# Performance work log

Hardware: AMD Instinct MI355X
Metric: run time of the kernel (lower is better)

The kernel has to match this reference:

```python
import jax, jax.numpy as jnp
import numpy as np

NREF, NALT, B, D, F = 131072, 32768, 4096, 128, 512
H = F // 2  # d_ffn // 2
EPS = 1e-5


def _ln(x, w, b):
    m = jnp.mean(x, axis=-1, keepdims=True)
    v = jnp.mean((x - m) ** 2, axis=-1, keepdims=True)
    return (x - m) * jax.lax.rsqrt(v + EPS) * w + b


def setup_inputs() -> dict:
    key = jax.random.key(0)
    ks = jax.random.split(key, 16)
    s = 0.02
    return {
        "ref_flat": jax.random.normal(ks[0], (NREF, D), jnp.float32),
        "alt_flat": jax.random.normal(ks[1], (NALT, D), jnp.float32),
        "ref_seg": jnp.sort(jax.random.randint(ks[2], (NREF,), 0, B)),
        "alt_seg": jnp.sort(jax.random.randint(ks[3], (NALT,), 0, B)),
        "norm1_w": jnp.ones((D,), jnp.float32),
        "norm1_b": jnp.zeros((D,), jnp.float32),
        "w1_ref": jax.random.normal(ks[4], (D, F), jnp.float32) * s,
        "b1_ref": jnp.zeros((F,), jnp.float32),
        "w1_alt": jax.random.normal(ks[5], (D, F), jnp.float32) * s,
        "b1_alt": jnp.zeros((F,), jnp.float32),
        "norm2_w": jnp.ones((H,), jnp.float32),
        "norm2_b": jnp.zeros((H,), jnp.float32),
        "alpha_ref": jnp.float32(0.01),
        "alpha_alt": jnp.float32(0.01),
        "beta_ref": jnp.float32(0.01),
        "beta_alt": jnp.float32(0.01),
        "gamma": jnp.float32(0.01),
        "ref_regularizer": 0.1 * jnp.ones((H,), jnp.float32),
        "reg_w_pre": jnp.float32(np.log(0.1)),
        "w2_ref": jax.random.normal(ks[6], (H, D), jnp.float32) * s,
        "b2_ref": jnp.zeros((D,), jnp.float32),
        "w2_alt": jax.random.normal(ks[7], (H, D), jnp.float32) * s,
        "b2_alt": jnp.zeros((D,), jnp.float32),
    }


def reference(ref_flat, alt_flat, ref_seg, alt_seg,
              norm1_w, norm1_b, w1_ref, b1_ref, w1_alt, b1_alt,
              norm2_w, norm2_b, alpha_ref, alpha_alt, beta_ref, beta_alt,
              gamma, ref_regularizer, reg_w_pre, w2_ref, b2_ref, w2_alt, b2_alt):
    # proj1 + SELU on flattened ragged reads
    zr = jax.nn.selu(_ln(ref_flat, norm1_w, norm1_b) @ w1_ref + b1_ref)   # [NREF, F]
    za = jax.nn.selu(_ln(alt_flat, norm1_w, norm1_b) @ w1_alt + b1_alt)   # [NALT, F]
    z1r, z2r = zr[:, :H], zr[:, H:]
    z1a, z2a = za[:, :H], za[:, H:]
    z2r = _ln(z2r, norm2_w, norm2_b)
    z2a = _ln(z2a, norm2_w, norm2_b)

    cnt_r = jax.ops.segment_sum(jnp.ones((NREF,), z2r.dtype), ref_seg, num_segments=B)
    cnt_a = jax.ops.segment_sum(jnp.ones((NALT,), z2a.dtype), alt_seg, num_segments=B)
    reg_w = jnp.exp(reg_w_pre) + 0.25
    # regularized mean field over each ref set
    ref_mf = (jax.ops.segment_sum(z2r, ref_seg, num_segments=B)
              + reg_w * ref_regularizer) / (cnt_r[:, None] + reg_w)       # [B, H]
    alt_mf = jax.ops.segment_sum(z2a, alt_seg, num_segments=B) \
             / jnp.maximum(cnt_a, 1.0)[:, None]                            # [B, H]

    ref_gate = z2r * alpha_ref + 1.0 + (beta_ref * ref_mf)[ref_seg]
    alt_gate = z2a * alpha_alt + 1.0 + (beta_alt * alt_mf + gamma * ref_mf)[alt_seg]

    out_r = ref_flat + (z1r * ref_gate) @ w2_ref + b2_ref
    out_a = alt_flat + (z1a * alt_gate) @ w2_alt + b2_alt
    return out_r, out_a
```

## Files before the change

### kernel.cpp

```cpp
#include <hip/hip_runtime.h>
#include <hip/hip_bf16.h>

#define NREF 131072
#define NALT 32768
#define BSEG 4096
#define D 128
#define F 512
#define H 256
#define EPS 1e-5f
#define NB_REF 4096
#define NB_ALT 1024

typedef short short8 __attribute__((ext_vector_type(8)));
typedef float f32x4 __attribute__((ext_vector_type(4)));

__device__ __forceinline__ float selu_f(float z) {
    const float sc = 1.0507009873554805f;
    const float al = 1.6732632423543772f;
    return z > 0.f ? sc * z : sc * al * (__expf(z) - 1.f);
}

__device__ __forceinline__ short f2bf(float v) {
    __bf16 b = (__bf16)v;
    return __builtin_bit_cast(short, b);
}

__device__ __forceinline__ float bf2f(short s) {
    return (float)__builtin_bit_cast(__bf16, s);
}

__global__ void prep_kernel(const float* __restrict__ w1_ref, const float* __restrict__ w1_alt,
                            const float* __restrict__ w2_ref, const float* __restrict__ w2_alt,
                            __bf16* __restrict__ w1p_r, __bf16* __restrict__ w1p_a,
                            __bf16* __restrict__ w2p_r, __bf16* __restrict__ w2p_a,
                            float* __restrict__ zbase) {
    int b = blockIdx.x;
    if (b < 768) {
        const float* w; __bf16* wp; int KT, N, idx;
        if (b < 256)      { w = w1_ref; wp = w1p_r; KT = 4; N = F; idx = b * 256 + threadIdx.x; }
        else if (b < 512) { w = w1_alt; wp = w1p_a; KT = 4; N = F; idx = (b - 256) * 256 + threadIdx.x; }
        else if (b < 640) { w = w2_ref; wp = w2p_r; KT = 8; N = D; idx = (b - 512) * 256 + threadIdx.x; }
        else              { w = w2_alt; wp = w2p_a; KT = 8; N = D; idx = (b - 640) * 256 + threadIdx.x; }
        int j = idx & 7;
        int l = (idx >> 3) & 63;
        int t = idx >> 9;
        int kt = t % KT;
        int nt = t / KT;
        int k = kt * 32 + ((l >> 4) << 3) + j;
        int n = (nt << 4) + (l & 15);
        wp[idx] = (__bf16)w[k * N + n];
    } else {
        int t = (b - 768) * 256 + threadIdx.x;
        float4 z = {0.f, 0.f, 0.f, 0.f};
        for (int i = t; i < 526336; i += 512 * 256)
            reinterpret_cast<float4*>(zbase)[i] = z;
    }
}

__global__ __launch_bounds__(256, 4)
void pass1_kernel(const float* __restrict__ xr_, const float* __restrict__ xa_,
                  const int* __restrict__ segr_, const int* __restrict__ sega_,
                  const __bf16* __restrict__ w1pr_, const __bf16* __restrict__ w1pa_,
                  const float* __restrict__ b1r_, const float* __restrict__ b1a_,
                  const float* __restrict__ n1w, const float* __restrict__ n1b,
                  const float* __restrict__ n2w, const float* __restrict__ n2b,
                  float* __restrict__ sumr_, float* __restrict__ cntr_,
                  float* __restrict__ suma_, float* __restrict__ cnta_,
                  __bf16* __restrict__ z2nr_, __bf16* __restrict__ z2na_,
                  int boff) {
    __shared__ __align__(16) __bf16 ys[32 * 128];
    __shared__ __align__(16) __bf16 z2s[32 * 256];
    __shared__ float n2w_s[H], n2b_s[H];
    __shared__ int seg_s[32];

    const int b = blockIdx.x + boff;
    const float* x; const int* seg; const __bf16* w1p; const float* b1;
    float* seg_sum; float* seg_cnt; __bf16* z2n_out; size_t row0;
    if (b < NB_REF) {
        x = xr_; seg = segr_; w1p = w1pr_; b1 = b1r_;
        seg_sum = sumr_; seg_cnt = cntr_; z2n_out = z2nr_;
        row0 = (size_t)b * 32;
    } else {
        x = xa_; seg = sega_; w1p = w1pa_; b1 = b1a_;
        seg_sum = suma_; seg_cnt = cnta_; z2n_out = z2na_;
        row0 = (size_t)(b - NB_REF) * 32;
    }

    const int tid = threadIdx.x;
    const int lane = tid & 63;
    const int wv = tid >> 6;
    const int q = lane >> 4, m0 = lane & 15;

    short8 bb[2][4];
    #pragma unroll
    for (int p = 0; p < 2; ++p)
        #pragma unroll
        for (int kt = 0; kt < 4; ++kt)
            bb[p][kt] = *reinterpret_cast<const short8*>(
                w1p + ((size_t)((16 + wv * 4 + p) * 4 + kt) * 64 + lane) * 8);
    float b1v[4];
    #pragma unroll
    for (int nt = 0; nt < 4; ++nt) b1v[nt] = b1[256 + (wv * 4 + nt) * 16 + m0];

    const int r = tid >> 3, g = tid & 7;
    float xr[16];
    #pragma unroll
    for (int i = 0; i < 4; ++i) {
        float4 t = *reinterpret_cast<const float4*>(x + (row0 + r) * D + g * 16 + i * 4);
        xr[i * 4 + 0] = t.x; xr[i * 4 + 1] = t.y; xr[i * 4 + 2] = t.z; xr[i * 4 + 3] = t.w;
    }
    float w1r[16], c1r[16];
    #pragma unroll
    for (int i = 0; i < 4; ++i) {
        float4 t = *reinterpret_cast<const float4*>(n1w + g * 16 + i * 4);
        w1r[i * 4 + 0] = t.x; w1r[i * 4 + 1] = t.y; w1r[i * 4 + 2] = t.z; w1r[i * 4 + 3] = t.w;
        float4 u = *reinterpret_cast<const float4*>(n1b + g * 16 + i * 4);
        c1r[i * 4 + 0] = u.x; c1r[i * 4 + 1] = u.y; c1r[i * 4 + 2] = u.z; c1r[i * 4 + 3] = u.w;
    }

    n2w_s[tid] = n2w[tid]; n2b_s[tid] = n2b[tid];
    if (tid < 32) seg_s[tid] = seg[row0 + tid];

    {
        float s = 0.f, ss = 0.f;
        #pragma unroll
        for (int i = 0; i < 16; ++i) { s += xr[i]; ss += xr[i] * xr[i]; }
        s += __shfl_xor(s, 1); ss += __shfl_xor(ss, 1);
        s += __shfl_xor(s, 2); ss += __shfl_xor(ss, 2);
        s += __shfl_xor(s, 4); ss += __shfl_xor(ss, 4);
        float mean = s * (1.f / 128.f);
        float var = ss * (1.f / 128.f) - mean * mean;
        float rsv = rsqrtf(var + EPS);
        const int swr = (r & 7) << 3;
        #pragma unroll
        for (int h = 0; h < 2; ++h) {
            short8 pk;
            #pragma unroll
            for (int j = 0; j < 8; ++j)
                pk[j] = f2bf((xr[h * 8 + j] - mean) * rsv * w1r[h * 8 + j] + c1r[h * 8 + j]);
            *reinterpret_cast<short8*>(&ys[r * 128 + ((g * 16 + h * 8) ^ swr)]) = pk;
        }
    }
    __syncthreads();

    {
        const int swm = (m0 & 7) << 3;
        const int ccol = q << 3;
        short8 a0[4], a1[4];
        #pragma unroll
        for (int kt = 0; kt < 4; ++kt) {
            a0[kt] = *reinterpret_cast<const short8*>(&ys[m0 * 128 + ((kt * 32 + ccol) ^ swm)]);
            a1[kt] = *reinterpret_cast<const short8*>(&ys[(m0 + 16) * 128 + ((kt * 32 + ccol) ^ swm)]);
        }
        #pragma unroll
        for (int nt = 0; nt < 4; ++nt) {
            f32x4 acc0 = {0.f, 0.f, 0.f, 0.f};
            f32x4 acc1 = {0.f, 0.f, 0.f, 0.f};
            #pragma unroll
            for (int kt = 0; kt < 4; ++kt) {
                acc0 = __builtin_amdgcn_mfma_f32_16x16x32_bf16(a0[kt], bb[nt & 1][kt], acc0, 0, 0, 0);
                acc1 = __builtin_amdgcn_mfma_f32_16x16x32_bf16(a1[kt], bb[nt & 1][kt], acc1, 0, 0, 0);
            }
            if (nt < 2) {
                #pragma unroll
                for (int kt = 0; kt < 4; ++kt)
                    bb[nt & 1][kt] = *reinterpret_cast<const short8*>(
                        w1p + ((size_t)((16 + wv * 4 + nt + 2) * 4 + kt) * 64 + lane) * 8);
            }
            int cz = (wv * 4 + nt) * 16 + m0;
            #pragma unroll
            for (int reg = 0; reg < 4; ++reg) {
                int r0 = (q << 2) + reg;
                int r1 = r0 + 16;
                z2s[r0 * 256 + (cz ^ ((r0 & 7) << 3))] = (__bf16)selu_f(acc0[reg] + b1v[nt]);
                z2s[r1 * 256 + (cz ^ ((r1 & 7) << 3))] = (__bf16)selu_f(acc1[reg] + b1v[nt]);
            }
        }
    }
    __syncthreads();

    {
        const int swr = (r & 7) << 3;
        float vb[32];
        float s2 = 0.f, q2 = 0.f;
        #pragma unroll
        for (int i = 0; i < 4; ++i) {
            short8 v = *reinterpret_cast<const short8*>(&z2s[r * 256 + ((g * 32 + i * 8) ^ swr)]);
            #pragma unroll
            for (int j = 0; j < 8; ++j) {
                float f = bf2f(v[j]);
                vb[i * 8 + j] = f; s2 += f; q2 += f * f;
            }
        }
        s2 += __shfl_xor(s2, 1); q2 += __shfl_xor(q2, 1);
        s2 += __shfl_xor(s2, 2); q2 += __shfl_xor(q2, 2);
        s2 += __shfl_xor(s2, 4); q2 += __shfl_xor(q2, 4);
        float mean2 = s2 * (1.f / 256.f);
        float var2 = q2 * (1.f / 256.f) - mean2 * mean2;
        float rs2 = rsqrtf(var2 + EPS);
        #pragma unroll
        for (int i = 0; i < 4; ++i) {
            short8 o;
            #pragma unroll
            for (int j = 0; j < 8; ++j) {
                int col = g * 32 + i * 8 + j;
                o[j] = f2bf((vb[i * 8 + j] - mean2) * rs2 * n2w_s[col] + n2b_s[col]);
            }
            *reinterpret_cast<short8*>(&z2s[r * 256 + ((g * 32 + i * 8) ^ swr)]) = o;
            *reinterpret_cast<short8*>(z2n_out + (row0 + r) * H + g * 32 + i * 8) = o;
        }
    }
    __syncthreads();

    {
        int c = tid;
        int s_cur = seg_s[0];
        float run = 0.f;
        for (int rr = 0; rr < 32; ++rr) {
            int sg = seg_s[rr];
            if (sg != s_cur) {
                atomicAdd(&seg_sum[(size_t)s_cur * H + c], run);
                run = 0.f; s_cur = sg;
            }
            run += (float)z2s[rr * 256 + (c ^ ((rr & 7) << 3))];
        }
        atomicAdd(&seg_sum[(size_t)s_cur * H + c], run);
        if (tid == 0) {
            int sc = seg_s[0]; float rl = 0.f;
            for (int rr = 0; rr < 32; ++rr) {
                if (seg_s[rr] != sc) { atomicAdd(&seg_cnt[sc], rl); rl = 0.f; sc = seg_s[rr]; }
                rl += 1.f;
            }
            atomicAdd(&seg_cnt[sc], rl);
        }
    }
}

__global__ void mf_kernel(const float* __restrict__ sum_r, const float* __restrict__ cnt_r,
                          const float* __restrict__ sum_a, const float* __restrict__ cnt_a,
                          const float* __restrict__ regz, const float* __restrict__ reg_w_pre,
                          const float* __restrict__ beta_ref, const float* __restrict__ beta_alt,
                          const float* __restrict__ gamma,
                          float* __restrict__ G_ref, float* __restrict__ G_alt) {
    int s = blockIdx.x, c = threadIdx.x;
    size_t i = (size_t)s * H + c;
    float rw = __expf(reg_w_pre[0]) + 0.25f;
    float mfr = (sum_r[i] + rw * regz[c]) / (cnt_r[s] + rw);
    float mfa = sum_a[i] / fmaxf(cnt_a[s], 1.f);
    G_ref[i] = beta_ref[0] * mfr;
    G_alt[i] = beta_alt[0] * mfa + gamma[0] * mfr;
}

__global__ __launch_bounds__(256, 4)
void pass2_kernel(const float* __restrict__ xr_, const float* __restrict__ xa_,
                  const int* __restrict__ segr_, const int* __restrict__ sega_,
                  const __bf16* __restrict__ w1pr_, const __bf16* __restrict__ w1pa_,
                  const float* __restrict__ b1r_, const float* __restrict__ b1a_,
                  const __bf16* __restrict__ w2pr_, const __bf16* __restrict__ w2pa_,
                  const float* __restrict__ b2r_, const float* __restrict__ b2a_,
                  const float* __restrict__ n1w, const float* __restrict__ n1b,
                  const float* __restrict__ alphar_, const float* __restrict__ alphaa_,
                  const float* __restrict__ Gr_, const float* __restrict__ Ga_,
                  const __bf16* __restrict__ z2nr_, const __bf16* __restrict__ z2na_,
                  float* __restrict__ out_, int boff) {
    __shared__ __align__(16) __bf16 ys[32 * 128];
    __shared__ __align__(16) __bf16 zs[32 * 256];

    const int b = blockIdx.x + boff;
    const float* x; const int* seg; const __bf16* w1p; const float* b1;
    const __bf16* w2p; const float* b2; const float* alpha_p; const float* G;
    const __bf16* z2n; float* out; size_t row0;
    if (b < NB_REF) {
        x = xr_; seg = segr_; w1p = w1pr_; b1 = b1r_; w2p = w2pr_; b2 = b2r_;
        alpha_p = alphar_; G = Gr_; z2n = z2nr_; out = out_;
        row0 = (size_t)b * 32;
    } else {
        x = xa_; seg = sega_; w1p = w1pa_; b1 = b1a_; w2p = w2pa_; b2 = b2a_;
        alpha_p = alphaa_; G = Ga_; z2n = z2na_; out = out_ + (size_t)NREF * D;
        row0 = (size_t)(b - NB_REF) * 32;
    }

    const int tid = threadIdx.x;
    const int lane = tid & 63;
    const int wv = tid >> 6;
    const int q = lane >> 4, m0 = lane & 15;
    const int r = tid >> 3, g = tid & 7;

    short8 bb[2][4];
    #pragma unroll
    for (int p = 0; p < 2; ++p)
        #pragma unroll
        for (int kt = 0; kt < 4; ++kt)
            bb[p][kt] = *reinterpret_cast<const short8*>(
                w1p + ((size_t)((wv * 4 + p) * 4 + kt) * 64 + lane) * 8);
    float b1v[4];
    #pragma unroll
    for (int nt = 0; nt < 4; ++nt) b1v[nt] = b1[(wv * 4 + nt) * 16 + m0];

    const int segi = seg[row0 + r];
    const float alpha = alpha_p[0];

    float xr[16];
    #pragma unroll
    for (int i = 0; i < 4; ++i) {
        float4 t = *reinterpret_cast<const float4*>(x + (row0 + r) * D + g * 16 + i * 4);
        xr[i * 4 + 0] = t.x; xr[i * 4 + 1] = t.y; xr[i * 4 + 2] = t.z; xr[i * 4 + 3] = t.w;
    }
    float w1r[16], c1r[16];
    #pragma unroll
    for (int i = 0; i < 4; ++i) {
        float4 t = *reinterpret_cast<const float4*>(n1w + g * 16 + i * 4);
        w1r[i * 4 + 0] = t.x; w1r[i * 4 + 1] = t.y; w1r[i * 4 + 2] = t.z; w1r[i * 4 + 3] = t.w;
        float4 u = *reinterpret_cast<const float4*>(n1b + g * 16 + i * 4);
        c1r[i * 4 + 0] = u.x; c1r[i * 4 + 1] = u.y; c1r[i * 4 + 2] = u.z; c1r[i * 4 + 3] = u.w;
    }

    {
        float s = 0.f, ss = 0.f;
        #pragma unroll
        for (int i = 0; i < 16; ++i) { s += xr[i]; ss += xr[i] * xr[i]; }
        s += __shfl_xor(s, 1); ss += __shfl_xor(ss, 1);
        s += __shfl_xor(s, 2); ss += __shfl_xor(ss, 2);
        s += __shfl_xor(s, 4); ss += __shfl_xor(ss, 4);
        float mean = s * (1.f / 128.f);
        float var = ss * (1.f / 128.f) - mean * mean;
        float rsv = rsqrtf(var + EPS);
        const int swr = (r & 7) << 3;
        #pragma unroll
        for (int h = 0; h < 2; ++h) {
            short8 pk;
            #pragma unroll
            for (int j = 0; j < 8; ++j)
                pk[j] = f2bf((xr[h * 8 + j] - mean) * rsv * w1r[h * 8 + j] + c1r[h * 8 + j]);
            *reinterpret_cast<short8*>(&ys[r * 128 + ((g * 16 + h * 8) ^ swr)]) = pk;
        }
    }
    __syncthreads();

    {
        const int swm = (m0 & 7) << 3;
        const int ccol = q << 3;
        short8 a0[4], a1[4];
        #pragma unroll
        for (int kt = 0; kt < 4; ++kt) {
            a0[kt] = *reinterpret_cast<const short8*>(&ys[m0 * 128 + ((kt * 32 + ccol) ^ swm)]);
            a1[kt] = *reinterpret_cast<const short8*>(&ys[(m0 + 16) * 128 + ((kt * 32 + ccol) ^ swm)]);
        }
        #pragma unroll
        for (int nt = 0; nt < 4; ++nt) {
            f32x4 acc0 = {0.f, 0.f, 0.f, 0.f};
            f32x4 acc1 = {0.f, 0.f, 0.f, 0.f};
            #pragma unroll
            for (int kt = 0; kt < 4; ++kt) {
                acc0 = __builtin_amdgcn_mfma_f32_16x16x32_bf16(a0[kt], bb[nt & 1][kt], acc0, 0, 0, 0);
                acc1 = __builtin_amdgcn_mfma_f32_16x16x32_bf16(a1[kt], bb[nt & 1][kt], acc1, 0, 0, 0);
            }
            if (nt < 2) {
                #pragma unroll
                for (int kt = 0; kt < 4; ++kt)
                    bb[nt & 1][kt] = *reinterpret_cast<const short8*>(
                        w1p + ((size_t)((wv * 4 + nt + 2) * 4 + kt) * 64 + lane) * 8);
            }
            int cz = (wv * 4 + nt) * 16 + m0;
            #pragma unroll
            for (int reg = 0; reg < 4; ++reg) {
                int r0 = (q << 2) + reg;
                int r1 = r0 + 16;
                zs[r0 * 256 + (cz ^ ((r0 & 7) << 3))] = (__bf16)selu_f(acc0[reg] + b1v[nt]);
                zs[r1 * 256 + (cz ^ ((r1 & 7) << 3))] = (__bf16)selu_f(acc1[reg] + b1v[nt]);
            }
        }
    }

    short8 zn[4];
    #pragma unroll
    for (int i = 0; i < 4; ++i)
        zn[i] = *reinterpret_cast<const short8*>(z2n + (row0 + r) * H + g * 32 + i * 8);
    float gvf[32];
    {
        const float* Gp = G + (size_t)segi * H + g * 32;
        #pragma unroll
        for (int i = 0; i < 8; ++i) {
            float4 t = *reinterpret_cast<const float4*>(Gp + i * 4);
            gvf[i * 4 + 0] = t.x; gvf[i * 4 + 1] = t.y; gvf[i * 4 + 2] = t.z; gvf[i * 4 + 3] = t.w;
        }
    }
    short8 b2f[2][8];
    #pragma unroll
    for (int p = 0; p < 2; ++p)
        #pragma unroll
        for (int kt = 0; kt < 8; ++kt)
            b2f[p][kt] = *reinterpret_cast<const short8*>(
                w2p + ((size_t)((wv * 2 + p) * 8 + kt) * 64 + lane) * 8);
    float b2v[2];
    #pragma unroll
    for (int p = 0; p < 2; ++p) b2v[p] = b2[(wv * 2 + p) * 16 + m0];
    __syncthreads();

    {
        const int swr = (r & 7) << 3;
        #pragma unroll
        for (int i = 0; i < 4; ++i) {
            int idx = r * 256 + ((g * 32 + i * 8) ^ swr);
            short8 v = *reinterpret_cast<const short8*>(&zs[idx]);
            short8 o;
            #pragma unroll
            for (int j = 0; j < 8; ++j) {
                float gate = bf2f(zn[i][j]) * alpha + 1.f + gvf[i * 8 + j];
                o[j] = f2bf(bf2f(v[j]) * gate);
            }
            *reinterpret_cast<short8*>(&zs[idx]) = o;
        }
    }
    float xres[16];
    #pragma unroll
    for (int p = 0; p < 2; ++p) {
        int col = (wv * 2 + p) * 16 + m0;
        #pragma unroll
        for (int reg = 0; reg < 4; ++reg) {
            int r0 = (q << 2) + reg;
            xres[p * 8 + reg]     = x[(row0 + r0) * D + col];
            xres[p * 8 + 4 + reg] = x[(row0 + r0 + 16) * D + col];
        }
    }
    __syncthreads();

    {
        const int swm = (m0 & 7) << 3;
        const int ccol = q << 3;
        f32x4 zero = {0.f, 0.f, 0.f, 0.f};
        f32x4 acc[2][2] = {{zero, zero}, {zero, zero}};
        #pragma unroll
        for (int kt = 0; kt < 8; ++kt) {
            short8 a0 = *reinterpret_cast<const short8*>(&zs[m0 * 256 + ((kt * 32 + ccol) ^ swm)]);
            short8 a1 = *reinterpret_cast<const short8*>(&zs[(m0 + 16) * 256 + ((kt * 32 + ccol) ^ swm)]);
            #pragma unroll
            for (int p = 0; p < 2; ++p) {
                acc[p][0] = __builtin_amdgcn_mfma_f32_16x16x32_bf16(a0, b2f[p][kt], acc[p][0], 0, 0, 0);
                acc[p][1] = __builtin_amdgcn_mfma_f32_16x16x32_bf16(a1, b2f[p][kt], acc[p][1], 0, 0, 0);
            }
        }
        #pragma unroll
        for (int p = 0; p < 2; ++p) {
            int col = (wv * 2 + p) * 16 + m0;
            #pragma unroll
            for (int reg = 0; reg < 4; ++reg) {
                int r0 = (q << 2) + reg;
                out[(row0 + r0) * D + col]      = acc[p][0][reg] + b2v[p] + xres[p * 8 + reg];
                out[(row0 + r0 + 16) * D + col] = acc[p][1][reg] + b2v[p] + xres[p * 8 + 4 + reg];
            }
        }
    }
}

extern "C" void kernel_launch(void* const* d_in, const int* in_sizes, int n_in,
                              void* d_out, int out_size, void* d_ws, size_t ws_size,
                              hipStream_t stream) {
    const float* ref_flat = (const float*)d_in[0];
    const float* alt_flat = (const float*)d_in[1];
    const int*   ref_seg  = (const int*)d_in[2];
    const int*   alt_seg  = (const int*)d_in[3];
    const float* norm1_w  = (const float*)d_in[4];
    const float* norm1_b  = (const float*)d_in[5];
    const float* w1_ref   = (const float*)d_in[6];
    const float* b1_ref   = (const float*)d_in[7];
    const float* w1_alt   = (const float*)d_in[8];
    const float* b1_alt   = (const float*)d_in[9];
    const float* norm2_w  = (const float*)d_in[10];
    const float* norm2_b  = (const float*)d_in[11];
    const float* alpha_ref = (const float*)d_in[12];
    const float* alpha_alt = (const float*)d_in[13];
    const float* beta_ref  = (const float*)d_in[14];
    const float* beta_alt  = (const float*)d_in[15];
    const float* gamma     = (const float*)d_in[16];
    const float* ref_regularizer = (const float*)d_in[17];
    const float* reg_w_pre = (const float*)d_in[18];
    const float* w2_ref   = (const float*)d_in[19];
    const float* b2_ref   = (const float*)d_in[20];
    const float* w2_alt   = (const float*)d_in[21];
    const float* b2_alt   = (const float*)d_in[22];

    char* ws = (char*)d_ws;
    float* sum_r = (float*)(ws);
    float* sum_a = (float*)(ws + 4194304);
    float* cnt_r = (float*)(ws + 8388608);
    float* cnt_a = (float*)(ws + 8404992);
    float* G_ref = (float*)(ws + 8421376);
    float* G_alt = (float*)(ws + 12615680);
    __bf16* w1p_r = (__bf16*)(ws + 16809984);
    __bf16* w1p_a = (__bf16*)(ws + 16941056);
    __bf16* w2p_r = (__bf16*)(ws + 17072128);
    __bf16* w2p_a = (__bf16*)(ws + 17137664);
    __bf16* z2n_r = (__bf16*)(ws + 17203200);
    __bf16* z2n_a = (__bf16*)(ws + 84312064);

    const bool merged = ws_size >= (size_t)101089280;
    if (!merged) z2n_a = z2n_r;

    prep_kernel<<<1280, 256, 0, stream>>>(w1_ref, w1_alt, w2_ref, w2_alt,
                                          w1p_r, w1p_a, w2p_r, w2p_a, (float*)ws);

    if (merged) {
        pass1_kernel<<<NB_REF + NB_ALT, 256, 0, stream>>>(
            ref_flat, alt_flat, ref_seg, alt_seg, w1p_r, w1p_a, b1_ref, b1_alt,
            norm1_w, norm1_b, norm2_w, norm2_b,
            sum_r, cnt_r, sum_a, cnt_a, z2n_r, z2n_a, 0);
        mf_kernel<<<BSEG, 256, 0, stream>>>(sum_r, cnt_r, sum_a, cnt_a,
                                            ref_regularizer, reg_w_pre,
                                            beta_ref, beta_alt, gamma, G_ref, G_alt);
        pass2_kernel<<<NB_REF + NB_ALT, 256, 0, stream>>>(
            ref_flat, alt_flat, ref_seg, alt_seg, w1p_r, w1p_a, b1_ref, b1_alt,
            w2p_r, w2p_a, b2_ref, b2_alt, norm1_w, norm1_b,
            alpha_ref, alpha_alt, G_ref, G_alt, z2n_r, z2n_a, (float*)d_out, 0);
    } else {
        pass1_kernel<<<NB_REF, 256, 0, stream>>>(
            ref_flat, alt_flat, ref_seg, alt_seg, w1p_r, w1p_a, b1_ref, b1_alt,
            norm1_w, norm1_b, norm2_w, norm2_b,
            sum_r, cnt_r, sum_a, cnt_a, z2n_r, z2n_a, 0);
        mf_kernel<<<BSEG, 256, 0, stream>>>(sum_r, cnt_r, sum_a, cnt_a,
                                            ref_regularizer, reg_w_pre,
                                            beta_ref, beta_alt, gamma, G_ref, G_alt);
        pass2_kernel<<<NB_REF, 256, 0, stream>>>(
            ref_flat, alt_flat, ref_seg, alt_seg, w1p_r, w1p_a, b1_ref, b1_alt,
            w2p_r, w2p_a, b2_ref, b2_alt, norm1_w, norm1_b,
            alpha_ref, alpha_alt, G_ref, G_alt, z2n_r, z2n_a, (float*)d_out, 0);
        pass1_kernel<<<NB_ALT, 256, 0, stream>>>(
            ref_flat, alt_flat, ref_seg, alt_seg, w1p_r, w1p_a, b1_ref, b1_alt,
            norm1_w, norm1_b, norm2_w, norm2_b,
            sum_r, cnt_r, sum_a, cnt_a, z2n_r, z2n_a, NB_REF);
        mf_kernel<<<BSEG, 256, 0, stream>>>(sum_r, cnt_r, sum_a, cnt_a,
                                            ref_regularizer, reg_w_pre,
                                            beta_ref, beta_alt, gamma, G_ref, G_alt);
        pass2_kernel<<<NB_ALT, 256, 0, stream>>>(
            ref_flat, alt_flat, ref_seg, alt_seg, w1p_r, w1p_a, b1_ref, b1_alt,
            w2p_r, w2p_a, b2_ref, b2_alt, norm1_w, norm1_b,
            alpha_ref, alpha_alt, G_ref, G_alt, z2n_r, z2n_a, (float*)d_out, NB_REF);
    }
}
```

Before: 300.3 us.

## Fuse mean-field kernel into pass2 and raise occupancy launch bounds

Removes the separate mf_kernel launch and computes the per-segment gate term inside pass2 directly from the segment sums, counts and regularizer. This drops one kernel launch plus the writes and reads of the two B×H G buffers, and shrinks the workspace. In exchange, each pass2 thread does extra loads and arithmetic: sum_r and regz for every row, and sum_a too for alt rows. Launch bounds for pass1 and pass2 also go from 4 to 6 waves-per-EU target, which may force register spills.

```diff
diff --git a/kernel.cpp b/kernel.cpp
--- a/kernel.cpp
+++ b/kernel.cpp
@@ -57,7 +57,7 @@
     }
 }
 
-__global__ __launch_bounds__(256, 4)
+__global__ __launch_bounds__(256, 6)
 void pass1_kernel(const float* __restrict__ xr_, const float* __restrict__ xa_,
                   const int* __restrict__ segr_, const int* __restrict__ sega_,
                   const __bf16* __restrict__ w1pr_, const __bf16* __restrict__ w1pa_,
@@ -236,22 +236,7 @@
     }
 }
 
-__global__ void mf_kernel(const float* __restrict__ sum_r, const float* __restrict__ cnt_r,
-                          const float* __restrict__ sum_a, const float* __restrict__ cnt_a,
-                          const float* __restrict__ regz, const float* __restrict__ reg_w_pre,
-                          const float* __restrict__ beta_ref, const float* __restrict__ beta_alt,
-                          const float* __restrict__ gamma,
-                          float* __restrict__ G_ref, float* __restrict__ G_alt) {
-    int s = blockIdx.x, c = threadIdx.x;
-    size_t i = (size_t)s * H + c;
-    float rw = __expf(reg_w_pre[0]) + 0.25f;
-    float mfr = (sum_r[i] + rw * regz[c]) / (cnt_r[s] + rw);
-    float mfa = sum_a[i] / fmaxf(cnt_a[s], 1.f);
-    G_ref[i] = beta_ref[0] * mfr;
-    G_alt[i] = beta_alt[0] * mfa + gamma[0] * mfr;
-}
-
-__global__ __launch_bounds__(256, 4)
+__global__ __launch_bounds__(256, 6)
 void pass2_kernel(const float* __restrict__ xr_, const float* __restrict__ xa_,
                   const int* __restrict__ segr_, const int* __restrict__ sega_,
                   const __bf16* __restrict__ w1pr_, const __bf16* __restrict__ w1pa_,
@@ -260,23 +245,28 @@
                   const float* __restrict__ b2r_, const float* __restrict__ b2a_,
                   const float* __restrict__ n1w, const float* __restrict__ n1b,
                   const float* __restrict__ alphar_, const float* __restrict__ alphaa_,
-                  const float* __restrict__ Gr_, const float* __restrict__ Ga_,
+                  const float* __restrict__ sum_r, const float* __restrict__ cnt_r,
+                  const float* __restrict__ sum_a, const float* __restrict__ cnt_a,
+                  const float* __restrict__ regz, const float* __restrict__ reg_w_pre,
+                  const float* __restrict__ beta_ref_p, const float* __restrict__ beta_alt_p,
+                  const float* __restrict__ gamma_p,
                   const __bf16* __restrict__ z2nr_, const __bf16* __restrict__ z2na_,
                   float* __restrict__ out_, int boff) {
     __shared__ __align__(16) __bf16 ys[32 * 128];
     __shared__ __align__(16) __bf16 zs[32 * 256];
 
     const int b = blockIdx.x + boff;
+    const bool isref = (b < NB_REF);
     const float* x; const int* seg; const __bf16* w1p; const float* b1;
-    const __bf16* w2p; const float* b2; const float* alpha_p; const float* G;
+    const __bf16* w2p; const float* b2; const float* alpha_p;
     const __bf16* z2n; float* out; size_t row0;
-    if (b < NB_REF) {
+    if (isref) {
         x = xr_; seg = segr_; w1p = w1pr_; b1 = b1r_; w2p = w2pr_; b2 = b2r_;
-        alpha_p = alphar_; G = Gr_; z2n = z2nr_; out = out_;
+        alpha_p = alphar_; z2n = z2nr_; out = out_;
         row0 = (size_t)b * 32;
     } else {
         x = xa_; seg = sega_; w1p = w1pa_; b1 = b1a_; w2p = w2pa_; b2 = b2a_;
-        alpha_p = alphaa_; G = Ga_; z2n = z2na_; out = out_ + (size_t)NREF * D;
+        alpha_p = alphaa_; z2n = z2na_; out = out_ + (size_t)NREF * D;
         row0 = (size_t)(b - NB_REF) * 32;
     }
 
@@ -299,6 +289,10 @@
 
     const int segi = seg[row0 + r];
     const float alpha = alpha_p[0];
+    const float rw = __expf(reg_w_pre[0]) + 0.25f;
+    const float bref = beta_ref_p[0];
+    const float balt = beta_alt_p[0];
+    const float gmma = gamma_p[0];
 
     float xr[16];
     #pragma unroll
@@ -378,11 +372,32 @@
         zn[i] = *reinterpret_cast<const short8*>(z2n + (row0 + r) * H + g * 32 + i * 8);
     float gvf[32];
     {
-        const float* Gp = G + (size_t)segi * H + g * 32;
-        #pragma unroll
-        for (int i = 0; i < 8; ++i) {
-            float4 t = *reinterpret_cast<const float4*>(Gp + i * 4);
-            gvf[i * 4 + 0] = t.x; gvf[i * 4 + 1] = t.y; gvf[i * 4 + 2] = t.z; gvf[i * 4 + 3] = t.w;
+        const float invr = 1.f / (cnt_r[segi] + rw);
+        const float* srow = sum_r + (size_t)segi * H + g * 32;
+        const float* rz = regz + g * 32;
+        if (isref) {
+            #pragma unroll
+            for (int i = 0; i < 8; ++i) {
+                float4 s4 = *reinterpret_cast<const float4*>(srow + i * 4);
+                float4 r4 = *reinterpret_cast<const float4*>(rz + i * 4);
+                gvf[i * 4 + 0] = bref * ((s4.x + rw * r4.x) * invr);
+                gvf[i * 4 + 1] = bref * ((s4.y + rw * r4.y) * invr);
+                gvf[i * 4 + 2] = bref * ((s4.z + rw * r4.z) * invr);
+                gvf[i * 4 + 3] = bref * ((s4.w + rw * r4.w) * invr);
+            }
+        } else {
+            const float inva = 1.f / fmaxf(cnt_a[segi], 1.f);
+            const float* sarow = sum_a + (size_t)segi * H + g * 32;
+            #pragma unroll
+            for (int i = 0; i < 8; ++i) {
+                float4 s4 = *reinterpret_cast<const float4*>(srow + i * 4);
+                float4 r4 = *reinterpret_cast<const float4*>(rz + i * 4);
+                float4 a4 = *reinterpret_cast<const float4*>(sarow + i * 4);
+                gvf[i * 4 + 0] = balt * (a4.x * inva) + gmma * ((s4.x + rw * r4.x) * invr);
+                gvf[i * 4 + 1] = balt * (a4.y * inva) + gmma * ((s4.y + rw * r4.y) * invr);
+                gvf[i * 4 + 2] = balt * (a4.z * inva) + gmma * ((s4.z + rw * r4.z) * invr);
+                gvf[i * 4 + 3] = balt * (a4.w * inva) + gmma * ((s4.w + rw * r4.w) * invr);
+            }
         }
     }
     short8 b2f[2][8];
@@ -485,16 +500,14 @@
     float* sum_a = (float*)(ws + 4194304);
     float* cnt_r = (float*)(ws + 8388608);
     float* cnt_a = (float*)(ws + 8404992);
-    float* G_ref = (float*)(ws + 8421376);
-    float* G_alt = (float*)(ws + 12615680);
-    __bf16* w1p_r = (__bf16*)(ws + 16809984);
-    __bf16* w1p_a = (__bf16*)(ws + 16941056);
-    __bf16* w2p_r = (__bf16*)(ws + 17072128);
-    __bf16* w2p_a = (__bf16*)(ws + 17137664);
-    __bf16* z2n_r = (__bf16*)(ws + 17203200);
-    __bf16* z2n_a = (__bf16*)(ws + 84312064);
-
-    const bool merged = ws_size >= (size_t)101089280;
+    __bf16* w1p_r = (__bf16*)(ws + 8421376);
+    __bf16* w1p_a = (__bf16*)(ws + 8552448);
+    __bf16* w2p_r = (__bf16*)(ws + 8683520);
+    __bf16* w2p_a = (__bf16*)(ws + 8749056);
+    __bf16* z2n_r = (__bf16*)(ws + 8814592);
+    __bf16* z2n_a = (__bf16*)(ws + 75923456);
+
+    const bool merged = ws_size >= (size_t)92700672;
     if (!merged) z2n_a = z2n_r;
 
     prep_kernel<<<1280, 256, 0, stream>>>(w1_ref, w1_alt, w2_ref, w2_alt,
@@ -505,35 +518,35 @@
             ref_flat, alt_flat, ref_seg, alt_seg, w1p_r, w1p_a, b1_ref, b1_alt,
             norm1_w, norm1_b, norm2_w, norm2_b,
             sum_r, cnt_r, sum_a, cnt_a, z2n_r, z2n_a, 0);
-        mf_kernel<<<BSEG, 256, 0, stream>>>(sum_r, cnt_r, sum_a, cnt_a,
-                                            ref_regularizer, reg_w_pre,
-                                            beta_ref, beta_alt, gamma, G_ref, G_alt);
         pass2_kernel<<<NB_REF + NB_ALT, 256, 0, stream>>>(
             ref_flat, alt_flat, ref_seg, alt_seg, w1p_r, w1p_a, b1_ref, b1_alt,
             w2p_r, w2p_a, b2_ref, b2_alt, norm1_w, norm1_b,
-            alpha_ref, alpha_alt, G_ref, G_alt, z2n_r, z2n_a, (float*)d_out, 0);
+            alpha_ref, alpha_alt,
+            sum_r, cnt_r, sum_a, cnt_a, ref_regularizer, reg_w_pre,
+            beta_ref, beta_alt, gamma,
+            z2n_r, z2n_a, (float*)d_out, 0);
     } else {
         pass1_kernel<<<NB_REF, 256, 0, stream>>>(
             ref_flat, alt_flat, ref_seg, alt_seg, w1p_r, w1p_a, b1_ref, b1_alt,
             norm1_w, norm1_b, norm2_w, norm2_b,
             sum_r, cnt_r, sum_a, cnt_a, z2n_r, z2n_a, 0);
-        mf_kernel<<<BSEG, 256, 0, stream>>>(sum_r, cnt_r, sum_a, cnt_a,
-                                            ref_regularizer, reg_w_pre,
-                                            beta_ref, beta_alt, gamma, G_ref, G_alt);
         pass2_kernel<<<NB_REF, 256, 0, stream>>>(
             ref_flat, alt_flat, ref_seg, alt_seg, w1p_r, w1p_a, b1_ref, b1_alt,
             w2p_r, w2p_a, b2_ref, b2_alt, norm1_w, norm1_b,
-            alpha_ref, alpha_alt, G_ref, G_alt, z2n_r, z2n_a, (float*)d_out, 0);
+            alpha_ref, alpha_alt,
+            sum_r, cnt_r, sum_a, cnt_a, ref_regularizer, reg_w_pre,
+            beta_ref, beta_alt, gamma,
+            z2n_r, z2n_a, (float*)d_out, 0);
         pass1_kernel<<<NB_ALT, 256, 0, stream>>>(
             ref_flat, alt_flat, ref_seg, alt_seg, w1p_r, w1p_a, b1_ref, b1_alt,
             norm1_w, norm1_b, norm2_w, norm2_b,
             sum_r, cnt_r, sum_a, cnt_a, z2n_r, z2n_a, NB_REF);
-        mf_kernel<<<BSEG, 256, 0, stream>>>(sum_r, cnt_r, sum_a, cnt_a,
-                                            ref_regularizer, reg_w_pre,
-                                            beta_ref, beta_alt, gamma, G_ref, G_alt);
         pass2_kernel<<<NB_ALT, 256, 0, stream>>>(
             ref_flat, alt_flat, ref_seg, alt_seg, w1p_r, w1p_a, b1_ref, b1_alt,
             w2p_r, w2p_a, b2_ref, b2_alt, norm1_w, norm1_b,
-            alpha_ref, alpha_alt, G_ref, G_alt, z2n_r, z2n_a, (float*)d_out, NB_REF);
-    }
-}
+            alpha_ref, alpha_alt,
+            sum_r, cnt_r, sum_a, cnt_a, ref_regularizer, reg_w_pre,
+            beta_ref, beta_alt, gamma,
+            z2n_r, z2n_a, (float*)d_out, NB_REF);
+    }
+}
```

Result: slower. 591.8 us (+97.1%).
